# Kernel tuning notes

Measured on AMD Instinct MI355X. Metric: run time of the kernel, lower is better.

The kernel has to match this reference:

```python
import jax, jax.numpy as jnp
import numpy as np

HIDDEN = 256
BATCH = 16
SEQ = 8192


def setup_inputs() -> dict:
    key = jax.random.key(0)
    k1, k2 = jax.random.split(key)
    x = jax.random.normal(k1, (BATCH, SEQ, HIDDEN), dtype=jnp.float32)
    # rotor_net parameters: Linear(hidden, hidden) followed by tanh
    W = jax.random.normal(k2, (HIDDEN, HIDDEN), dtype=jnp.float32) / np.sqrt(HIDDEN)
    b = jnp.zeros((HIDDEN,), dtype=jnp.float32)
    return {"x": x, "W": W, "b": b}


def reference(x, W, b):
    # Original torch code loops over subseq_size=10 chunks of the flattened
    # (B*S, H) tokens, applying rotor_net to each chunk and concatenating.
    # rotor_net is row-wise (Linear + tanh), so chunked application is
    # mathematically identical to one batched application over all tokens.
    B, S, H = x.shape
    flat = x.reshape(-1, H)                      # (B*S, H)
    out = jnp.tanh(flat @ W.T + b)               # (B*S, H)
    return out.reshape(B, S, -1)
```

## Files before the change

kernel.cpp:

```cpp
#include <hip/hip_runtime.h>
#include <hip/hip_bf16.h>


#define HIDDEN 256
#define M_TOTAL (16 * 8192)

using bf16x8 = __attribute__((ext_vector_type(8))) __bf16;
using bf16x4 = __attribute__((ext_vector_type(4))) __bf16;
using f32x4  = __attribute__((ext_vector_type(4))) float;

__device__ __forceinline__ bf16x4 cvt4(float4 v) {
    bf16x4 r;
    r[0] = (__bf16)v.x; r[1] = (__bf16)v.y;
    r[2] = (__bf16)v.z; r[3] = (__bf16)v.w;
    return r;
}

__global__ __launch_bounds__(256, 3) void rotor_kernel(const float* __restrict__ X,
                                                       const float* __restrict__ W,
                                                       const float* __restrict__ bias,
                                                       float* __restrict__ Y) {
    __shared__ __align__(16) unsigned char lds_raw[49152];
    __bf16* sW = (__bf16*)lds_raw;
    __bf16* sX = (__bf16*)(lds_raw + 32768);
    float*  sO = (float*)lds_raw;

    const int tid  = threadIdx.x;
    const int wave = tid >> 6, lane = tid & 63;
    const int q = lane >> 4, lr = lane & 15;

    const int g   = blockIdx.x;
    const int x8  = g & 7;
    const int h   = g >> 3;
    const int nb  = h & 3;
    const int mb  = (h >> 2) * 8 + x8;
    const int row0 = mb * 128;
    const int nbg  = nb * 64;

    {
        const int wr = tid >> 3;
        const int wk = (tid & 7) * 4;
        const int qw = (tid & 7) >> 1;
        const int lo = tid & 1;
#pragma unroll
        for (int j = 0; j < 2; ++j) {
            const int C = j * 32 + wr;
            const float* wsrc = W + (size_t)(nbg + C) * HIDDEN + wk;
            float4 t[8];
#pragma unroll
            for (int kc = 0; kc < 8; ++kc) t[kc] = *(const float4*)(wsrc + kc * 32);
            __bf16* wb = sW + (C >> 4) * 512 + (qw * 16 + (C & 15)) * 8 + lo * 4;
#pragma unroll
            for (int kc = 0; kc < 8; ++kc) *(bf16x4*)(wb + kc * 2048) = cvt4(t[kc]);
        }
    }

    const int xr8 = lane >> 3;
    const int qx  = (lane & 7) >> 1;
    const int lox = lane & 1;
    const float* xsrc = X + (size_t)(row0 + wave * 32 + xr8) * HIDDEN + (lane & 7) * 4;
    __bf16* xwb = sX + wave * 2048;

    float4 xr[4];
#pragma unroll
    for (int j = 0; j < 4; ++j) xr[j] = *(const float4*)(xsrc + (size_t)j * 8 * HIDDEN);
#pragma unroll
    for (int j = 0; j < 4; ++j) {
        const int R = j * 8 + xr8;
        *(bf16x4*)(xwb + (R >> 4) * 512 + (qx * 16 + (R & 15)) * 8 + lox * 4) = cvt4(xr[j]);
    }

    __syncthreads();

    f32x4 acc[2][4];
#pragma unroll
    for (int m = 0; m < 2; ++m)
#pragma unroll
        for (int t = 0; t < 4; ++t)
            acc[m][t] = (f32x4){0.f, 0.f, 0.f, 0.f};

    const __bf16* ard = sX + wave * 2048 + lane * 8;
    const __bf16* brd = sW + lane * 8;

#pragma unroll
    for (int c = 0; c < 8; ++c) {
        if (c < 7) {
#pragma unroll
            for (int j = 0; j < 4; ++j)
                xr[j] = *(const float4*)(xsrc + (size_t)j * 8 * HIDDEN + (c + 1) * 32);
        }
        const int bsel = (c & 1) * 1024;
        bf16x8 a0 = *(const bf16x8*)(ard + bsel);
        bf16x8 a1 = *(const bf16x8*)(ard + bsel + 512);
        bf16x8 b0 = *(const bf16x8*)(brd + (c * 4 + 0) * 512);
        bf16x8 b1 = *(const bf16x8*)(brd + (c * 4 + 1) * 512);
        bf16x8 b2 = *(const bf16x8*)(brd + (c * 4 + 2) * 512);
        bf16x8 b3 = *(const bf16x8*)(brd + (c * 4 + 3) * 512);

        acc[0][0] = __builtin_amdgcn_mfma_f32_16x16x32_bf16(a0, b0, acc[0][0], 0, 0, 0);
        acc[0][1] = __builtin_amdgcn_mfma_f32_16x16x32_bf16(a0, b1, acc[0][1], 0, 0, 0);
        acc[0][2] = __builtin_amdgcn_mfma_f32_16x16x32_bf16(a0, b2, acc[0][2], 0, 0, 0);
        acc[0][3] = __builtin_amdgcn_mfma_f32_16x16x32_bf16(a0, b3, acc[0][3], 0, 0, 0);
        acc[1][0] = __builtin_amdgcn_mfma_f32_16x16x32_bf16(a1, b0, acc[1][0], 0, 0, 0);
        acc[1][1] = __builtin_amdgcn_mfma_f32_16x16x32_bf16(a1, b1, acc[1][1], 0, 0, 0);
        acc[1][2] = __builtin_amdgcn_mfma_f32_16x16x32_bf16(a1, b2, acc[1][2], 0, 0, 0);
        acc[1][3] = __builtin_amdgcn_mfma_f32_16x16x32_bf16(a1, b3, acc[1][3], 0, 0, 0);

        if (c < 7) {
            const int nb2 = ((c + 1) & 1) * 1024;
#pragma unroll
            for (int j = 0; j < 4; ++j) {
                const int R = j * 8 + xr8;
                *(bf16x4*)(xwb + nb2 + (R >> 4) * 512 + (qx * 16 + (R & 15)) * 8 + lox * 4) = cvt4(xr[j]);
            }
        }
    }

    float bv[4];
#pragma unroll
    for (int t = 0; t < 4; ++t) bv[t] = bias[nbg + t * 16 + lr];

    float ov[2][4][4];
#pragma unroll
    for (int m = 0; m < 2; ++m)
#pragma unroll
        for (int t = 0; t < 4; ++t)
#pragma unroll
            for (int r = 0; r < 4; ++r) {
                float z = acc[m][t][r] + bv[t];
                z = fminf(fmaxf(z, -10.f), 10.f);
                const float e2 = __expf(2.0f * z);
                ov[m][t][r] = __fdividef(e2 - 1.0f, e2 + 1.0f);
            }

    __syncthreads();

    float* so = sO + wave * 2112;
#pragma unroll
    for (int m = 0; m < 2; ++m)
#pragma unroll
        for (int t = 0; t < 4; ++t)
#pragma unroll
            for (int r = 0; r < 4; ++r)
                so[(m * 16 + q * 4 + r) * 66 + t * 16 + lr] = ov[m][t][r];

    float* ybase = Y + (size_t)(row0 + wave * 32) * HIDDEN + nbg;
#pragma unroll
    for (int j = 0; j < 4; ++j) {
#pragma unroll
        for (int hh = 0; hh < 2; ++hh) {
            const int R = j * 8 + xr8;
            float4 v = *(const float4*)(so + R * 66 + hh * 32 + (lane & 7) * 4);
            *(float4*)(ybase + (size_t)R * HIDDEN + hh * 32 + (lane & 7) * 4) = v;
        }
    }
}

extern "C" void kernel_launch(void* const* d_in, const int* in_sizes, int n_in,
                              void* d_out, int out_size, void* d_ws, size_t ws_size,
                              hipStream_t stream) {
    const float* X    = (const float*)d_in[0];
    const float* W    = (const float*)d_in[1];
    const float* bias = (const float*)d_in[2];
    float* Y          = (float*)d_out;

    rotor_kernel<<<dim3((M_TOTAL / 128) * (HIDDEN / 64)), dim3(256), 0, stream>>>(X, W, bias, Y);
}
```

Baseline: 264.6 us.

## Pre-pack W into MFMA fragments and stream B operands from global memory

Adds a small prologue kernel that converts W to bf16 and stores it in MFMA-fragment order in the workspace. The main kernel then loads B fragments straight from global memory, double-buffered in registers, instead of staging all of W in shared memory per block. Each wave keeps only a private LDS region, which removes both __syncthreads and cuts LDS to about 17KB so occupancy can rise to 4 blocks. The price is an extra kernel launch and repeated global/L2 reads of W fragments by every wave.

```diff
diff --git a/kernel.cpp b/kernel.cpp
--- a/kernel.cpp
+++ b/kernel.cpp
@@ -16,61 +16,63 @@
     return r;
 }
 
-__global__ __launch_bounds__(256, 3) void rotor_kernel(const float* __restrict__ X,
-                                                       const float* __restrict__ W,
+__global__ __launch_bounds__(256) void wfrag_kernel(const float* __restrict__ W,
+                                                    __bf16* __restrict__ WF) {
+    const int gid  = blockIdx.x * 256 + threadIdx.x;
+    const int lane = gid & 63;
+    const int t    = (gid >> 6) & 3;
+    const int c    = (gid >> 8) & 7;
+    const int nb   = gid >> 11;
+    const int lr = lane & 15, q = lane >> 4;
+    const float* src = W + (size_t)(nb * 64 + t * 16 + lr) * HIDDEN + c * 32 + q * 8;
+    float4 lo = *(const float4*)src;
+    float4 hi = *(const float4*)(src + 4);
+    bf16x8 v;
+    v[0] = (__bf16)lo.x; v[1] = (__bf16)lo.y; v[2] = (__bf16)lo.z; v[3] = (__bf16)lo.w;
+    v[4] = (__bf16)hi.x; v[5] = (__bf16)hi.y; v[6] = (__bf16)hi.z; v[7] = (__bf16)hi.w;
+    *(bf16x8*)(WF + (size_t)gid * 8) = v;
+}
+
+__global__ __launch_bounds__(256, 4) void rotor_kernel(const float* __restrict__ X,
+                                                       const __bf16* __restrict__ WF,
                                                        const float* __restrict__ bias,
                                                        float* __restrict__ Y) {
-    __shared__ __align__(16) unsigned char lds_raw[49152];
-    __bf16* sW = (__bf16*)lds_raw;
-    __bf16* sX = (__bf16*)(lds_raw + 32768);
-    float*  sO = (float*)lds_raw;
+    __shared__ __align__(16) unsigned char lds_raw[4 * 4352];
+    unsigned char* my = lds_raw + (threadIdx.x >> 6) * 4352;
+    __bf16* sX = (__bf16*)my;
+    float*  sO = (float*)my;
 
-    const int tid  = threadIdx.x;
-    const int wave = tid >> 6, lane = tid & 63;
+    const int lane = threadIdx.x & 63;
+    const int wave = threadIdx.x >> 6;
     const int q = lane >> 4, lr = lane & 15;
 
     const int g   = blockIdx.x;
     const int x8  = g & 7;
     const int h   = g >> 3;
-    const int nb  = h & 3;
+    const int nbi = h & 3;
     const int mb  = (h >> 2) * 8 + x8;
-    const int row0 = mb * 128;
-    const int nbg  = nb * 64;
+    const int row0 = mb * 128 + wave * 32;
+    const int nbg  = nbi * 64;
 
-    {
-        const int wr = tid >> 3;
-        const int wk = (tid & 7) * 4;
-        const int qw = (tid & 7) >> 1;
-        const int lo = tid & 1;
+    const int xr8 = lane >> 3, qx = (lane & 7) >> 1, lox = lane & 1;
+    const float* xsrc = X + (size_t)(row0 + xr8) * HIDDEN + (lane & 7) * 4;
+    int woff[4];
 #pragma unroll
-        for (int j = 0; j < 2; ++j) {
-            const int C = j * 32 + wr;
-            const float* wsrc = W + (size_t)(nbg + C) * HIDDEN + wk;
-            float4 t[8];
-#pragma unroll
-            for (int kc = 0; kc < 8; ++kc) t[kc] = *(const float4*)(wsrc + kc * 32);
-            __bf16* wb = sW + (C >> 4) * 512 + (qw * 16 + (C & 15)) * 8 + lo * 4;
-#pragma unroll
-            for (int kc = 0; kc < 8; ++kc) *(bf16x4*)(wb + kc * 2048) = cvt4(t[kc]);
-        }
+    for (int j = 0; j < 4; ++j) {
+        const int R = j * 8 + xr8;
+        woff[j] = (R >> 4) * 512 + (qx * 16 + (R & 15)) * 8 + lox * 4;
     }
 
-    const int xr8 = lane >> 3;
-    const int qx  = (lane & 7) >> 1;
-    const int lox = lane & 1;
-    const float* xsrc = X + (size_t)(row0 + wave * 32 + xr8) * HIDDEN + (lane & 7) * 4;
-    __bf16* xwb = sX + wave * 2048;
+    const __bf16* wf = WF + (size_t)nbi * (8 * 4 * 512) + lane * 8;
 
     float4 xr[4];
+    bf16x8 bc[4], bn[4];
 #pragma unroll
     for (int j = 0; j < 4; ++j) xr[j] = *(const float4*)(xsrc + (size_t)j * 8 * HIDDEN);
 #pragma unroll
-    for (int j = 0; j < 4; ++j) {
-        const int R = j * 8 + xr8;
-        *(bf16x4*)(xwb + (R >> 4) * 512 + (qx * 16 + (R & 15)) * 8 + lox * 4) = cvt4(xr[j]);
-    }
-
-    __syncthreads();
+    for (int t = 0; t < 4; ++t) bc[t] = *(const bf16x8*)(wf + t * 512);
+#pragma unroll
+    for (int j = 0; j < 4; ++j) *(bf16x4*)(sX + woff[j]) = cvt4(xr[j]);
 
     f32x4 acc[2][4];
 #pragma unroll
@@ -79,40 +81,35 @@
         for (int t = 0; t < 4; ++t)
             acc[m][t] = (f32x4){0.f, 0.f, 0.f, 0.f};
 
-    const __bf16* ard = sX + wave * 2048 + lane * 8;
-    const __bf16* brd = sW + lane * 8;
-
 #pragma unroll
     for (int c = 0; c < 8; ++c) {
         if (c < 7) {
 #pragma unroll
             for (int j = 0; j < 4; ++j)
                 xr[j] = *(const float4*)(xsrc + (size_t)j * 8 * HIDDEN + (c + 1) * 32);
+#pragma unroll
+            for (int t = 0; t < 4; ++t)
+                bn[t] = *(const bf16x8*)(wf + ((c + 1) * 4 + t) * 512);
         }
-        const int bsel = (c & 1) * 1024;
-        bf16x8 a0 = *(const bf16x8*)(ard + bsel);
-        bf16x8 a1 = *(const bf16x8*)(ard + bsel + 512);
-        bf16x8 b0 = *(const bf16x8*)(brd + (c * 4 + 0) * 512);
-        bf16x8 b1 = *(const bf16x8*)(brd + (c * 4 + 1) * 512);
-        bf16x8 b2 = *(const bf16x8*)(brd + (c * 4 + 2) * 512);
-        bf16x8 b3 = *(const bf16x8*)(brd + (c * 4 + 3) * 512);
+        const __bf16* ab = sX + (c & 1) * 1024 + lane * 8;
+        bf16x8 a0 = *(const bf16x8*)ab;
+        bf16x8 a1 = *(const bf16x8*)(ab + 512);
 
-        acc[0][0] = __builtin_amdgcn_mfma_f32_16x16x32_bf16(a0, b0, acc[0][0], 0, 0, 0);
-        acc[0][1] = __builtin_amdgcn_mfma_f32_16x16x32_bf16(a0, b1, acc[0][1], 0, 0, 0);
-        acc[0][2] = __builtin_amdgcn_mfma_f32_16x16x32_bf16(a0, b2, acc[0][2], 0, 0, 0);
-        acc[0][3] = __builtin_amdgcn_mfma_f32_16x16x32_bf16(a0, b3, acc[0][3], 0, 0, 0);
-        acc[1][0] = __builtin_amdgcn_mfma_f32_16x16x32_bf16(a1, b0, acc[1][0], 0, 0, 0);
-        acc[1][1] = __builtin_amdgcn_mfma_f32_16x16x32_bf16(a1, b1, acc[1][1], 0, 0, 0);
-        acc[1][2] = __builtin_amdgcn_mfma_f32_16x16x32_bf16(a1, b2, acc[1][2], 0, 0, 0);
-        acc[1][3] = __builtin_amdgcn_mfma_f32_16x16x32_bf16(a1, b3, acc[1][3], 0, 0, 0);
+        acc[0][0] = __builtin_amdgcn_mfma_f32_16x16x32_bf16(a0, bc[0], acc[0][0], 0, 0, 0);
+        acc[0][1] = __builtin_amdgcn_mfma_f32_16x16x32_bf16(a0, bc[1], acc[0][1], 0, 0, 0);
+        acc[0][2] = __builtin_amdgcn_mfma_f32_16x16x32_bf16(a0, bc[2], acc[0][2], 0, 0, 0);
+        acc[0][3] = __builtin_amdgcn_mfma_f32_16x16x32_bf16(a0, bc[3], acc[0][3], 0, 0, 0);
+        acc[1][0] = __builtin_amdgcn_mfma_f32_16x16x32_bf16(a1, bc[0], acc[1][0], 0, 0, 0);
+        acc[1][1] = __builtin_amdgcn_mfma_f32_16x16x32_bf16(a1, bc[1], acc[1][1], 0, 0, 0);
+        acc[1][2] = __builtin_amdgcn_mfma_f32_16x16x32_bf16(a1, bc[2], acc[1][2], 0, 0, 0);
+        acc[1][3] = __builtin_amdgcn_mfma_f32_16x16x32_bf16(a1, bc[3], acc[1][3], 0, 0, 0);
 
         if (c < 7) {
-            const int nb2 = ((c + 1) & 1) * 1024;
 #pragma unroll
-            for (int j = 0; j < 4; ++j) {
-                const int R = j * 8 + xr8;
-                *(bf16x4*)(xwb + nb2 + (R >> 4) * 512 + (qx * 16 + (R & 15)) * 8 + lox * 4) = cvt4(xr[j]);
-            }
+            for (int j = 0; j < 4; ++j)
+                *(bf16x4*)(sX + ((c + 1) & 1) * 1024 + woff[j]) = cvt4(xr[j]);
+#pragma unroll
+            for (int t = 0; t < 4; ++t) bc[t] = bn[t];
         }
     }
 
@@ -120,9 +117,9 @@
 #pragma unroll
     for (int t = 0; t < 4; ++t) bv[t] = bias[nbg + t * 16 + lr];
 
-    float ov[2][4][4];
+    float* yb = Y + (size_t)row0 * HIDDEN + nbg;
 #pragma unroll
-    for (int m = 0; m < 2; ++m)
+    for (int m = 0; m < 2; ++m) {
 #pragma unroll
         for (int t = 0; t < 4; ++t)
 #pragma unroll
@@ -130,28 +127,12 @@
                 float z = acc[m][t][r] + bv[t];
                 z = fminf(fmaxf(z, -10.f), 10.f);
                 const float e2 = __expf(2.0f * z);
-                ov[m][t][r] = __fdividef(e2 - 1.0f, e2 + 1.0f);
+                sO[(q * 4 + r) * 68 + t * 16 + lr] = __fdividef(e2 - 1.0f, e2 + 1.0f);
             }
-
-    __syncthreads();
-
-    float* so = sO + wave * 2112;
 #pragma unroll
-    for (int m = 0; m < 2; ++m)
-#pragma unroll
-        for (int t = 0; t < 4; ++t)
-#pragma unroll
-            for (int r = 0; r < 4; ++r)
-                so[(m * 16 + q * 4 + r) * 66 + t * 16 + lr] = ov[m][t][r];
-
-    float* ybase = Y + (size_t)(row0 + wave * 32) * HIDDEN + nbg;
-#pragma unroll
-    for (int j = 0; j < 4; ++j) {
-#pragma unroll
-        for (int hh = 0; hh < 2; ++hh) {
-            const int R = j * 8 + xr8;
-            float4 v = *(const float4*)(so + R * 66 + hh * 32 + (lane & 7) * 4);
-            *(float4*)(ybase + (size_t)R * HIDDEN + hh * 32 + (lane & 7) * 4) = v;
+        for (int j = 0; j < 4; ++j) {
+            float4 v = *(const float4*)(sO + (j * 4 + q) * 68 + lr * 4);
+            *(float4*)(yb + (size_t)(m * 16 + j * 4 + q) * HIDDEN + lr * 4) = v;
         }
     }
 }
@@ -163,6 +144,8 @@
     const float* W    = (const float*)d_in[1];
     const float* bias = (const float*)d_in[2];
     float* Y          = (float*)d_out;
+    __bf16* WF        = (__bf16*)d_ws;
 
-    rotor_kernel<<<dim3((M_TOTAL / 128) * (HIDDEN / 64)), dim3(256), 0, stream>>>(X, W, bias, Y);
+    wfrag_kernel<<<dim3(32), dim3(256), 0, stream>>>(W, WF);
+    rotor_kernel<<<dim3((M_TOTAL / 128) * (HIDDEN / 64)), dim3(256), 0, stream>>>(X, WF, bias, Y);
 }
```

New measurement: 258.8 us. -2.2%, faster.
